# Performance work log

Hardware: AMD Instinct MI355X
Metric: run time of the kernel (lower is better)

## Reference

```python
import jax, jax.numpy as jnp
import numpy as np

N = 100000   # nodes
E = 1600000  # edges (avg degree 16)
D = 64       # in_dim
H = 64       # hidden_dim
NEG_SLOPE = 0.2


def setup_inputs() -> dict:
    key = jax.random.key(0)
    ks = jax.random.split(key, 10)
    s = 0.1  # param init scale
    return {
        "x": jax.random.normal(ks[0], (N, D), jnp.float32),
        "edge_index": jax.random.randint(ks[1], (2, E), 0, N, dtype=jnp.int64),
        "h": jax.random.normal(ks[2], (1, N, H), jnp.float32),
        "c": jax.random.normal(ks[3], (1, N, H), jnp.float32),
        "W_gat": jax.random.normal(ks[4], (D, H), jnp.float32) * s,
        "att_src": jax.random.normal(ks[5], (H,), jnp.float32) * s,
        "att_dst": jax.random.normal(ks[6], (H,), jnp.float32) * s,
        "bias_gat": jax.random.normal(ks[7], (H,), jnp.float32) * s,
        "W_ih": jax.random.normal(ks[8], (4 * H, H), jnp.float32) * s,
        "W_hh": jax.random.normal(ks[9], (4 * H, H), jnp.float32) * s,
    }


def reference(x, edge_index, h, c, W_gat, att_src, att_dst, bias_gat, W_ih, W_hh):
    src, dst = edge_index[0], edge_index[1]  # message j -> i

    # ---- Breadth: GATConv (heads=1) + tanh ----
    xs = x @ W_gat                             # [N, H] projected features
    a_src = xs @ att_src                       # [N]
    a_dst = xs @ att_dst                       # [N]
    e = jax.nn.leaky_relu(a_src[src] + a_dst[dst], NEG_SLOPE)  # [E]
    # scatter-softmax over incoming edges of each destination node
    m = jax.lax.stop_gradient(jax.ops.segment_max(e, dst, num_segments=N))
    p = jnp.exp(e - m[dst])
    z = jax.ops.segment_sum(p, dst, num_segments=N)
    alpha = p / (z[dst] + 1e-16)               # [E]
    agg = jax.ops.segment_sum(xs[src] * alpha[:, None], dst, num_segments=N)
    xb = jnp.tanh(agg + bias_gat)              # [N, H]

    # ---- Depth: single-step bias-free LSTM ----
    h0, c0 = h[0], c[0]                        # [N, H]
    gates = xb @ W_ih.T + h0 @ W_hh.T          # [N, 4H]
    i, f, g, o = jnp.split(gates, 4, axis=-1)  # torch gate order i,f,g,o
    c1 = jax.nn.sigmoid(f) * c0 + jax.nn.sigmoid(i) * jnp.tanh(g)
    h1 = jax.nn.sigmoid(o) * jnp.tanh(c1)
    return h1, h1[None], c1[None]
```

## Files before the change

### kernel.cpp

```cpp
#include <hip/hip_runtime.h>
#include <cmath>

#define NN 100000
#define EE 1600000
#define NB 1563
#define CAP 1344
#define EPB 25

using bf16x8 = __attribute__((ext_vector_type(8))) __bf16;
using f32x4  = __attribute__((ext_vector_type(4))) float;

__device__ __forceinline__ unsigned short f2bf(float f) {
  __bf16 b = (__bf16)f;
  return __builtin_bit_cast(unsigned short, b);
}
__device__ __forceinline__ float bflo(unsigned int u) {
  return __uint_as_float(u << 16);
}
__device__ __forceinline__ float bfhi(unsigned int u) {
  return __uint_as_float(u & 0xffff0000u);
}
__device__ __forceinline__ float sigmoidf_(float v) {
  return 1.0f / (1.0f + __expf(-v));
}
__device__ __forceinline__ float tanhfast(float v) {
  return 1.0f - 2.0f / (1.0f + __expf(2.0f * v));
}
__device__ __forceinline__ bf16x8 cvt8(float4 a, float4 b) {
  bf16x8 r;
  r[0]=(__bf16)a.x; r[1]=(__bf16)a.y; r[2]=(__bf16)a.z; r[3]=(__bf16)a.w;
  r[4]=(__bf16)b.x; r[5]=(__bf16)b.y; r[6]=(__bf16)b.z; r[7]=(__bf16)b.w;
  return r;
}

__global__ __launch_bounds__(128) void k_prep(
    const float* __restrict__ Wih, const float* __restrict__ Whh,
    const float* __restrict__ Wg,
    unsigned short* __restrict__ wperm, unsigned short* __restrict__ wgp)
{
  if (blockIdx.x < 256) {
    const int p = blockIdx.x, k = threadIdx.x;
    const int g = p & 3;
    const int h = (p >> 4) + ((p >> 2) & 3) * 16;
    const int row = g*64 + h;
    const float v = (k < 64) ? Wih[row*64 + k] : Whh[row*64 + (k - 64)];
    wperm[p*128 + k] = f2bf(v);
  } else {
    for (int idx = threadIdx.x; idx < 4096; idx += 128) {
      const int lane = idx >> 6, r = idx & 63;
      const int nt = r >> 4, kf = (r >> 3) & 1, j = r & 7;
      const int m = lane & 15, quad = lane >> 4;
      wgp[idx] = f2bf(Wg[(kf*32 + quad*8 + j)*64 + nt*16 + m]);
    }
  }
}

__global__ __launch_bounds__(256) void k_binproj(
    const int* __restrict__ ei, int* __restrict__ bcursor,
    unsigned int* __restrict__ binned,
    const float* __restrict__ x, const unsigned short* __restrict__ wgp,
    const float* __restrict__ att_s, const float* __restrict__ att_d,
    unsigned short* __restrict__ xs16, float* __restrict__ a_src,
    float* __restrict__ a_dst)
{
  if (blockIdx.x < 256) {
    __shared__ int cnt[NB];
    __shared__ int gbase[NB];
    const int tid = threadIdx.x;
    const size_t base = (size_t)blockIdx.x * 256 * EPB;

    for (int b = tid; b < NB; b += 256) cnt[b] = 0;
    __syncthreads();

    unsigned int pay[EPB];
    int bidx[EPB], pos[EPB];
    #pragma unroll
    for (int j = 0; j < EPB; ++j) {
      const size_t e = base + (size_t)j*256 + tid;
      if (e < EE) {
        const int s = ei[e];
        const int d = ei[EE + e];
        bidx[j] = d >> 6;
        pay[j] = (unsigned)s | ((unsigned)(d & 63) << 17);
        pos[j] = atomicAdd(&cnt[bidx[j]], 1);
      } else {
        bidx[j] = -1;
      }
    }
    __syncthreads();

    for (int b = tid; b < NB; b += 256) {
      const int c = cnt[b];
      gbase[b] = c ? atomicAdd(&bcursor[b*16], c) : 0;
    }
    __syncthreads();

    #pragma unroll
    for (int j = 0; j < EPB; ++j) {
      if (bidx[j] >= 0) {
        const int g = gbase[bidx[j]] + pos[j];
        if (g < CAP) binned[(size_t)bidx[j]*CAP + g] = pay[j];
      }
    }
  } else {
    const int lane = threadIdx.x & 63;
    const int wave = threadIdx.x >> 6;
    const int tile = (blockIdx.x - 256) * 4 + wave;
    if (tile >= NN / 16) return;
    const int m = lane & 15, quad = lane >> 4;

    bf16x8 bfrag[4][2];
    {
      const unsigned short* wp = wgp + lane*64;
      #pragma unroll
      for (int nt = 0; nt < 4; ++nt)
        #pragma unroll
        for (int kf = 0; kf < 2; ++kf)
          bfrag[nt][kf] = *(const bf16x8*)(wp + nt*16 + kf*8);
    }

    const int row = tile*16 + m;
    bf16x8 afrag[2];
    #pragma unroll
    for (int kf = 0; kf < 2; ++kf) {
      const float4* p = (const float4*)(x + (size_t)row*64 + kf*32 + quad*8);
      afrag[kf] = cvt8(p[0], p[1]);
    }

    f32x4 acc[4];
    #pragma unroll
    for (int nt = 0; nt < 4; ++nt) acc[nt] = f32x4{0.f, 0.f, 0.f, 0.f};
    #pragma unroll
    for (int nt = 0; nt < 4; ++nt)
      #pragma unroll
      for (int kf = 0; kf < 2; ++kf)
        acc[nt] = __builtin_amdgcn_mfma_f32_16x16x32_bf16(
            afrag[kf], bfrag[nt][kf], acc[nt], 0, 0, 0);

    float ss[4] = {0.f,0.f,0.f,0.f}, sd[4] = {0.f,0.f,0.f,0.f};
    #pragma unroll
    for (int nt = 0; nt < 4; ++nt) {
      const float av = att_s[nt*16 + m], dv = att_d[nt*16 + m];
      #pragma unroll
      for (int r = 0; r < 4; ++r) {
        const float v = acc[nt][r];
        xs16[(size_t)(tile*16 + quad*4 + r)*64 + nt*16 + m] = f2bf(v);
        ss[r] += v * av;
        sd[r] += v * dv;
      }
    }
    #pragma unroll
    for (int off = 1; off < 16; off <<= 1) {
      #pragma unroll
      for (int r = 0; r < 4; ++r) {
        ss[r] += __shfl_xor(ss[r], off);
        sd[r] += __shfl_xor(sd[r], off);
      }
    }
    if (m == 0) {
      #pragma unroll
      for (int r = 0; r < 4; ++r) {
        a_src[tile*16 + quad*4 + r] = ss[r];
        a_dst[tile*16 + quad*4 + r] = sd[r];
      }
    }
  }
}

__global__ __launch_bounds__(256) void k_agg(
    const int* __restrict__ bcursor, const unsigned int* __restrict__ binned,
    const float* __restrict__ a_src, const float* __restrict__ a_dst,
    const unsigned short* __restrict__ xs16, const float* __restrict__ bias,
    unsigned short* __restrict__ xb16)
{
  __shared__ unsigned int raw[CAP];
  __shared__ unsigned int csr[CAP];
  __shared__ int cnt[64], offs[64], cursor[64];
  const int b = blockIdx.x;
  const int tid = threadIdx.x;
  const int ne = min(bcursor[b*16], CAP);

  if (tid < 64) cnt[tid] = 0;
  __syncthreads();
  for (int i = tid; i < ne; i += 256) {
    const unsigned int w = binned[(size_t)b*CAP + i];
    raw[i] = w;
    atomicAdd(&cnt[(w >> 17) & 63], 1);
  }
  __syncthreads();
  if (tid < 64) {
    const int v = cnt[tid];
    int inc = v;
    #pragma unroll
    for (int dd = 1; dd < 64; dd <<= 1) {
      const int o = __shfl_up(inc, dd, 64);
      if (tid >= dd) inc += o;
    }
    offs[tid] = inc - v;
    cursor[tid] = inc - v;
  }
  __syncthreads();
  for (int i = tid; i < ne; i += 256) {
    const unsigned int w = raw[i];
    const int pos = atomicAdd(&cursor[(w >> 17) & 63], 1);
    csr[pos] = w;
  }
  __syncthreads();

  const int lane = tid & 63;
  const int wv = tid >> 6;
  const int grp = lane >> 4, l16 = lane & 15;
  const float4 b4 = *(const float4*)(bias + l16*4);
  for (int t = 0; t < 16; ++t) {
    const int nl = wv*16 + t;
    const int node = b*64 + nl;
    if (node >= NN) break;
    const int bse = offs[nl];
    const int dg = cnt[nl];
    const float ad = a_dst[node];
    float acc0=0.f, acc1=0.f, acc2=0.f, acc3=0.f, psum=0.f;
    for (int e = grp; e < dg; e += 4) {
      const int s = (int)(csr[bse + e] & 0x1FFFFu);
      float ev = a_src[s] + ad;
      ev = (ev >= 0.f) ? ev : 0.2f*ev;
      const float pv = __expf(ev);
      const uint2 rw = *(const uint2*)(xs16 + (size_t)s*64 + l16*4);
      psum += pv;
      acc0 += pv*bflo(rw.x); acc1 += pv*bfhi(rw.x);
      acc2 += pv*bflo(rw.y); acc3 += pv*bfhi(rw.y);
    }
    #pragma unroll
    for (int off = 16; off < 64; off <<= 1) {
      acc0 += __shfl_xor(acc0, off);
      acc1 += __shfl_xor(acc1, off);
      acc2 += __shfl_xor(acc2, off);
      acc3 += __shfl_xor(acc3, off);
      psum += __shfl_xor(psum, off);
    }
    if (lane < 16) {
      const float invz = 1.f/(psum + 1e-16f);
      ushort4 o;
      o.x = f2bf(tanhfast(acc0*invz + b4.x));
      o.y = f2bf(tanhfast(acc1*invz + b4.y));
      o.z = f2bf(tanhfast(acc2*invz + b4.z));
      o.w = f2bf(tanhfast(acc3*invz + b4.w));
      *(ushort4*)(xb16 + (size_t)node*64 + l16*4) = o;
    }
  }
}

__global__ __launch_bounds__(256) void k_lstm(
    const unsigned short* __restrict__ xb16, const float* __restrict__ h0,
    const float* __restrict__ c0, const unsigned short* __restrict__ wperm,
    float* __restrict__ out)
{
  const int lane = threadIdx.x & 63;
  const int wv = threadIdx.x >> 6;
  const int m = lane & 15, quad = lane >> 4;

  bf16x8 wfr[4][4];
  #pragma unroll
  for (int u = 0; u < 4; ++u) {
    const unsigned short* wr = wperm + (size_t)((wv*4 + u)*16 + m)*128;
    #pragma unroll
    for (int kf = 0; kf < 4; ++kf)
      wfr[u][kf] = *(const bf16x8*)(wr + kf*32 + quad*8);
  }

  for (int tile = blockIdx.x; tile < NN/16; tile += gridDim.x) {
    const int node = tile*16 + m;
    const size_t obase = (size_t)node*64 + quad*16 + wv*4;
    const float4 cv = *(const float4*)(c0 + obase);

    bf16x8 bfr[4];
    bfr[0] = *(const bf16x8*)(xb16 + (size_t)node*64 + quad*8);
    bfr[1] = *(const bf16x8*)(xb16 + (size_t)node*64 + 32 + quad*8);
    {
      const float* p0 = h0 + (size_t)node*64 + quad*8;
      bfr[2] = cvt8(*(const float4*)p0, *(const float4*)(p0 + 4));
      const float* p1 = h0 + (size_t)node*64 + 32 + quad*8;
      bfr[3] = cvt8(*(const float4*)p1, *(const float4*)(p1 + 4));
    }

    f32x4 acc[4];
    #pragma unroll
    for (int u = 0; u < 4; ++u) acc[u] = f32x4{0.f, 0.f, 0.f, 0.f};
    #pragma unroll
    for (int u = 0; u < 4; ++u)
      #pragma unroll
      for (int kf = 0; kf < 4; ++kf)
        acc[u] = __builtin_amdgcn_mfma_f32_16x16x32_bf16(
            wfr[u][kf], bfr[kf], acc[u], 0, 0, 0);

    const float cvv[4] = {cv.x, cv.y, cv.z, cv.w};
    float h1a[4], c1a[4];
    #pragma unroll
    for (int u = 0; u < 4; ++u) {
      const float gi = acc[u][0], gf = acc[u][1];
      const float gg = acc[u][2], go = acc[u][3];
      const float c1 = sigmoidf_(gf)*cvv[u] + sigmoidf_(gi)*tanhfast(gg);
      h1a[u] = sigmoidf_(go)*tanhfast(c1);
      c1a[u] = c1;
    }
    const float4 hv  = make_float4(h1a[0], h1a[1], h1a[2], h1a[3]);
    const float4 c1v = make_float4(c1a[0], c1a[1], c1a[2], c1a[3]);
    *(float4*)(out + obase) = hv;
    *(float4*)(out + (size_t)NN*64 + obase) = hv;
    *(float4*)(out + (size_t)2*NN*64 + obase) = c1v;
  }
}

extern "C" void kernel_launch(void* const* d_in, const int* in_sizes, int n_in,
                              void* d_out, int out_size, void* d_ws, size_t ws_size,
                              hipStream_t stream) {
  const float* x    = (const float*)d_in[0];
  const int*   ei   = (const int*)d_in[1];
  const float* h    = (const float*)d_in[2];
  const float* c    = (const float*)d_in[3];
  const float* Wg   = (const float*)d_in[4];
  const float* atts = (const float*)d_in[5];
  const float* attd = (const float*)d_in[6];
  const float* bg   = (const float*)d_in[7];
  const float* Wih  = (const float*)d_in[8];
  const float* Whh  = (const float*)d_in[9];
  float* out = (float*)d_out;

  char* w = (char*)d_ws;
  unsigned short* xs16  = (unsigned short*)w; w += (size_t)NN*64*2;
  unsigned short* xb16  = (unsigned short*)w; w += (size_t)NN*64*2;
  unsigned short* wperm = (unsigned short*)w; w += (size_t)256*128*2;
  unsigned short* wgp   = (unsigned short*)w; w += (size_t)4096*2;
  unsigned int*   binned= (unsigned int*)w;  w += (size_t)NB*CAP*4;
  float* a_src = (float*)w; w += (size_t)NN*4;
  float* a_dst = (float*)w; w += (size_t)NN*4;
  int* bcursor = (int*)w;   w += (size_t)NB*16*4;

  hipMemsetAsync(bcursor, 0, (size_t)NB*16*4, stream);

  k_prep    <<<257, 128, 0, stream>>>(Wih, Whh, Wg, wperm, wgp);
  k_binproj <<<256 + (NN/16 + 3)/4, 256, 0, stream>>>(
      ei, bcursor, binned, x, wgp, atts, attd, xs16, a_src, a_dst);
  k_agg     <<<NB, 256, 0, stream>>>(bcursor, binned, a_src, a_dst, xs16, bg, xb16);
  k_lstm    <<<2084, 256, 0, stream>>>(xb16, h, c, wperm, out);
}
```

Before: 305.6 us.

## Pre-convert h0 to bf16 and stage swizzled LSTM weights in LDS

Extra blocks in the binning/projection kernel now convert h0 from fp32 to bf16 ahead of time, so the LSTM kernel reads half the bytes for h. The LSTM kernel switches to 1024-thread blocks that copy the whole 64 KB permuted weight matrix into LDS with an XOR swizzle to avoid bank conflicts. Each wave then does one tile, with no grid-stride loop. This trades per-wave register weight loads for shared-memory reads plus an extra h16 write and read pass. The large LDS footprint may limit occupancy.

Result: faster. 288.6 us (-5.6%).

```diff
diff --git a/kernel.cpp b/kernel.cpp
--- a/kernel.cpp
+++ b/kernel.cpp
@@ -6,6 +6,9 @@
 #define NB 1563
 #define CAP 1344
 #define EPB 25
+#define NTILE 6250
+#define PROJB 1563
+#define CVTB 3125
 
 using bf16x8 = __attribute__((ext_vector_type(8))) __bf16;
 using f32x4  = __attribute__((ext_vector_type(4))) float;
@@ -44,7 +47,8 @@
     const int h = (p >> 4) + ((p >> 2) & 3) * 16;
     const int row = g*64 + h;
     const float v = (k < 64) ? Wih[row*64 + k] : Whh[row*64 + (k - 64)];
-    wperm[p*128 + k] = f2bf(v);
+    const int gp = (k >> 3) ^ (p & 15);
+    wperm[p*128 + gp*8 + (k & 7)] = f2bf(v);
   } else {
     for (int idx = threadIdx.x; idx < 4096; idx += 128) {
       const int lane = idx >> 6, r = idx & 63;
@@ -61,7 +65,8 @@
     const float* __restrict__ x, const unsigned short* __restrict__ wgp,
     const float* __restrict__ att_s, const float* __restrict__ att_d,
     unsigned short* __restrict__ xs16, float* __restrict__ a_src,
-    float* __restrict__ a_dst)
+    float* __restrict__ a_dst,
+    const float* __restrict__ h0, unsigned short* __restrict__ h16)
 {
   if (blockIdx.x < 256) {
     __shared__ int cnt[NB];
@@ -102,11 +107,11 @@
         if (g < CAP) binned[(size_t)bidx[j]*CAP + g] = pay[j];
       }
     }
-  } else {
+  } else if (blockIdx.x < 256 + PROJB) {
     const int lane = threadIdx.x & 63;
     const int wave = threadIdx.x >> 6;
     const int tile = (blockIdx.x - 256) * 4 + wave;
-    if (tile >= NN / 16) return;
+    if (tile >= NTILE) return;
     const int m = lane & 15, quad = lane >> 4;
 
     bf16x8 bfrag[4][2];
@@ -164,6 +169,11 @@
         a_dst[tile*16 + quad*4 + r] = sd[r];
       }
     }
+  } else {
+    const int idx = (blockIdx.x - 256 - PROJB)*256 + threadIdx.x;
+    const float* p = h0 + (size_t)idx*8;
+    const bf16x8 v = cvt8(*(const float4*)p, *(const float4*)(p + 4));
+    *(bf16x8*)(h16 + (size_t)idx*8) = v;
   }
 }
 
@@ -249,65 +259,75 @@
   }
 }
 
-__global__ __launch_bounds__(256) void k_lstm(
-    const unsigned short* __restrict__ xb16, const float* __restrict__ h0,
+__global__ __launch_bounds__(1024, 2) void k_lstm(
+    const unsigned short* __restrict__ xb16, const unsigned short* __restrict__ h16,
     const float* __restrict__ c0, const unsigned short* __restrict__ wperm,
     float* __restrict__ out)
 {
-  const int lane = threadIdx.x & 63;
-  const int wv = threadIdx.x >> 6;
+  __shared__ unsigned short wlds[256*128];
+  const int tid = threadIdx.x;
+  {
+    const float4* gs = (const float4*)wperm;
+    float4* ls = (float4*)wlds;
+    #pragma unroll
+    for (int i = 0; i < 4; ++i) ls[tid + i*1024] = gs[tid + i*1024];
+  }
+  __syncthreads();
+
+  const int w = tid >> 6, lane = tid & 63;
+  const int wv = w & 3, tsub = w >> 2;
   const int m = lane & 15, quad = lane >> 4;
-
-  bf16x8 wfr[4][4];
+  const int tile = blockIdx.x*4 + tsub;
+  if (tile >= NTILE) return;
+  const int node = tile*16 + m;
+
+  bf16x8 bfr[4];
+  bfr[0] = *(const bf16x8*)(xb16 + (size_t)node*64 + quad*8);
+  bfr[1] = *(const bf16x8*)(xb16 + (size_t)node*64 + 32 + quad*8);
+  bfr[2] = *(const bf16x8*)(h16 + (size_t)node*64 + quad*8);
+  bfr[3] = *(const bf16x8*)(h16 + (size_t)node*64 + 32 + quad*8);
+
+  const int q32 = (m >> 2) & 3;
+  const int base = (wv*64 + m)*256 + ((quad ^ (m & 3)) << 4);
+  const char* lb = (const char*)wlds;
+  const int a0 = base + ((0 ^ q32) << 6);
+  const int a1 = base + ((1 ^ q32) << 6);
+  const int a2 = base + ((2 ^ q32) << 6);
+  const int a3 = base + ((3 ^ q32) << 6);
+
+  f32x4 acc[4];
+  #pragma unroll
+  for (int u = 0; u < 4; ++u) acc[u] = f32x4{0.f, 0.f, 0.f, 0.f};
   #pragma unroll
   for (int u = 0; u < 4; ++u) {
-    const unsigned short* wr = wperm + (size_t)((wv*4 + u)*16 + m)*128;
-    #pragma unroll
-    for (int kf = 0; kf < 4; ++kf)
-      wfr[u][kf] = *(const bf16x8*)(wr + kf*32 + quad*8);
-  }
-
-  for (int tile = blockIdx.x; tile < NN/16; tile += gridDim.x) {
-    const int node = tile*16 + m;
-    const size_t obase = (size_t)node*64 + quad*16 + wv*4;
-    const float4 cv = *(const float4*)(c0 + obase);
-
-    bf16x8 bfr[4];
-    bfr[0] = *(const bf16x8*)(xb16 + (size_t)node*64 + quad*8);
-    bfr[1] = *(const bf16x8*)(xb16 + (size_t)node*64 + 32 + quad*8);
-    {
-      const float* p0 = h0 + (size_t)node*64 + quad*8;
-      bfr[2] = cvt8(*(const float4*)p0, *(const float4*)(p0 + 4));
-      const float* p1 = h0 + (size_t)node*64 + 32 + quad*8;
-      bfr[3] = cvt8(*(const float4*)p1, *(const float4*)(p1 + 4));
-    }
-
-    f32x4 acc[4];
-    #pragma unroll
-    for (int u = 0; u < 4; ++u) acc[u] = f32x4{0.f, 0.f, 0.f, 0.f};
-    #pragma unroll
-    for (int u = 0; u < 4; ++u)
-      #pragma unroll
-      for (int kf = 0; kf < 4; ++kf)
-        acc[u] = __builtin_amdgcn_mfma_f32_16x16x32_bf16(
-            wfr[u][kf], bfr[kf], acc[u], 0, 0, 0);
-
-    const float cvv[4] = {cv.x, cv.y, cv.z, cv.w};
-    float h1a[4], c1a[4];
-    #pragma unroll
-    for (int u = 0; u < 4; ++u) {
-      const float gi = acc[u][0], gf = acc[u][1];
-      const float gg = acc[u][2], go = acc[u][3];
-      const float c1 = sigmoidf_(gf)*cvv[u] + sigmoidf_(gi)*tanhfast(gg);
-      h1a[u] = sigmoidf_(go)*tanhfast(c1);
-      c1a[u] = c1;
-    }
-    const float4 hv  = make_float4(h1a[0], h1a[1], h1a[2], h1a[3]);
-    const float4 c1v = make_float4(c1a[0], c1a[1], c1a[2], c1a[3]);
-    *(float4*)(out + obase) = hv;
-    *(float4*)(out + (size_t)NN*64 + obase) = hv;
-    *(float4*)(out + (size_t)2*NN*64 + obase) = c1v;
-  }
+    const int uo = u*4096;
+    const bf16x8 w0 = *(const bf16x8*)(lb + a0 + uo);
+    const bf16x8 w1 = *(const bf16x8*)(lb + a1 + uo);
+    const bf16x8 w2 = *(const bf16x8*)(lb + a2 + uo);
+    const bf16x8 w3 = *(const bf16x8*)(lb + a3 + uo);
+    acc[u] = __builtin_amdgcn_mfma_f32_16x16x32_bf16(w0, bfr[0], acc[u], 0, 0, 0);
+    acc[u] = __builtin_amdgcn_mfma_f32_16x16x32_bf16(w1, bfr[1], acc[u], 0, 0, 0);
+    acc[u] = __builtin_amdgcn_mfma_f32_16x16x32_bf16(w2, bfr[2], acc[u], 0, 0, 0);
+    acc[u] = __builtin_amdgcn_mfma_f32_16x16x32_bf16(w3, bfr[3], acc[u], 0, 0, 0);
+  }
+
+  const size_t obase = (size_t)node*64 + quad*16 + wv*4;
+  const float4 cv = *(const float4*)(c0 + obase);
+  const float cvv[4] = {cv.x, cv.y, cv.z, cv.w};
+  float h1a[4], c1a[4];
+  #pragma unroll
+  for (int u = 0; u < 4; ++u) {
+    const float gi = acc[u][0], gf = acc[u][1];
+    const float gg = acc[u][2], go = acc[u][3];
+    const float c1 = sigmoidf_(gf)*cvv[u] + sigmoidf_(gi)*tanhfast(gg);
+    h1a[u] = sigmoidf_(go)*tanhfast(c1);
+    c1a[u] = c1;
+  }
+  const float4 hv  = make_float4(h1a[0], h1a[1], h1a[2], h1a[3]);
+  const float4 c1v = make_float4(c1a[0], c1a[1], c1a[2], c1a[3]);
+  *(float4*)(out + obase) = hv;
+  *(float4*)(out + (size_t)NN*64 + obase) = hv;
+  *(float4*)(out + (size_t)2*NN*64 + obase) = c1v;
 }
 
 extern "C" void kernel_launch(void* const* d_in, const int* in_sizes, int n_in,
@@ -328,6 +348,7 @@
   char* w = (char*)d_ws;
   unsigned short* xs16  = (unsigned short*)w; w += (size_t)NN*64*2;
   unsigned short* xb16  = (unsigned short*)w; w += (size_t)NN*64*2;
+  unsigned short* h16   = (unsigned short*)w; w += (size_t)NN*64*2;
   unsigned short* wperm = (unsigned short*)w; w += (size_t)256*128*2;
   unsigned short* wgp   = (unsigned short*)w; w += (size_t)4096*2;
   unsigned int*   binned= (unsigned int*)w;  w += (size_t)NB*CAP*4;
@@ -338,8 +359,8 @@
   hipMemsetAsync(bcursor, 0, (size_t)NB*16*4, stream);
 
   k_prep    <<<257, 128, 0, stream>>>(Wih, Whh, Wg, wperm, wgp);
-  k_binproj <<<256 + (NN/16 + 3)/4, 256, 0, stream>>>(
-      ei, bcursor, binned, x, wgp, atts, attd, xs16, a_src, a_dst);
+  k_binproj <<<256 + PROJB + CVTB, 256, 0, stream>>>(
+      ei, bcursor, binned, x, wgp, atts, attd, xs16, a_src, a_dst, h, h16);
   k_agg     <<<NB, 256, 0, stream>>>(bcursor, binned, a_src, a_dst, xs16, bg, xb16);
-  k_lstm    <<<2084, 256, 0, stream>>>(xb16, h, c, wperm, out);
-}
+  k_lstm    <<<PROJB, 1024, 0, stream>>>(xb16, h16, c, wperm, out);
+}
```
